# Performance work log

Measured on AMD Instinct MI355X. Metric: run time of the kernel, lower is better.

Reference implementation:

```python
import jax, jax.numpy as jnp
import numpy as np

B, Hh, Ww, E = 8, 32, 32, 256
HEADS = 8
KD = E // HEADS  # 32
FFN = 1024
NQ = 64
SCALING = KD ** -0.5
EPS = 1e-6


def _ln(x, g, b):
    m = x.mean(-1, keepdims=True)
    v = ((x - m) ** 2).mean(-1, keepdims=True)
    return (x - m) * jax.lax.rsqrt(v + EPS) * g + b


def _dwconv(x, w, b, pad):
    # x: (b,h,w,c); w: (c,1,kh,kw) depthwise
    y = jnp.transpose(x, (0, 3, 1, 2))
    y = jax.lax.conv_general_dilated(
        y, w, (1, 1), [(pad, pad), (pad, pad)],
        dimension_numbers=('NCHW', 'OIHW', 'NCHW'),
        feature_group_count=y.shape[1])
    y = y + b[None, :, None, None]
    return jnp.transpose(y, (0, 2, 3, 1))


def _rot2(x):
    x1 = x[..., ::2]
    x2 = x[..., 1::2]
    return jnp.stack([-x2, x1], axis=-1).reshape(x.shape)


def _theta_shift(x, sin, cos):
    return x * cos + _rot2(x) * sin


def _ffn(x, fc1_w, fc1_b, fc2_w, fc2_b):
    h = jax.nn.gelu(x @ fc1_w.T + fc1_b, approximate=False)
    return h @ fc2_w.T + fc2_b


def _mha(q, k, v, in_w, in_b, out_w, out_b):
    # torch nn.MultiheadAttention, batch_first=True
    wq, wk, wv = in_w[:E], in_w[E:2 * E], in_w[2 * E:]
    bq, bk, bv = in_b[:E], in_b[E:2 * E], in_b[2 * E:]
    b_, nq, _ = q.shape
    lk = k.shape[1]
    qp = (q @ wq.T + bq).reshape(b_, nq, HEADS, KD).transpose(0, 2, 1, 3)
    kp = (k @ wk.T + bk).reshape(b_, lk, HEADS, KD).transpose(0, 2, 1, 3)
    vp = (v @ wv.T + bv).reshape(b_, lk, HEADS, KD).transpose(0, 2, 1, 3)
    att = jax.nn.softmax(jnp.einsum('bhqd,bhkd->bhqk', qp, kp) * SCALING, axis=-1)
    out = jnp.einsum('bhqk,bhkd->bhqd', att, vp)
    out = out.transpose(0, 2, 1, 3).reshape(b_, nq, E)
    return out @ out_w.T + out_b


def setup_inputs() -> dict:
    key = jax.random.key(0)
    ks = jax.random.split(key, 24)
    n = lambda i, shp, s=1.0: jax.random.normal(ks[i], shp, jnp.float32) * s
    W = 0.02
    return {
        'x': n(0, (B, Hh, Ww, E)),
        'queries': n(1, (B, NQ, E)),
        'sin': n(2, (Hh, Ww, KD)),
        'cos': n(3, (Hh, Ww, KD)),
        'mask': n(4, (HEADS, Hh * Ww, Hh * Ww)),
        'ln1_g': jnp.ones((E,), jnp.float32), 'ln1_b': jnp.zeros((E,), jnp.float32),
        'ln2_g': jnp.ones((E,), jnp.float32), 'ln2_b': jnp.zeros((E,), jnp.float32),
        'wq': n(5, (E, E), W), 'bq': jnp.zeros((E,), jnp.float32),
        'wk': n(6, (E, E), W), 'bk': jnp.zeros((E,), jnp.float32),
        'wv': n(7, (E, E), W), 'bv': jnp.zeros((E,), jnp.float32),
        'lepe_w': n(8, (E, 1, 5, 5), W), 'lepe_b': jnp.zeros((E,), jnp.float32),
        'wo': n(9, (E, E), W), 'bo': jnp.zeros((E,), jnp.float32),
        'fc1_w': n(10, (FFN, E), W), 'fc1_b': jnp.zeros((FFN,), jnp.float32),
        'fc2_w': n(11, (E, FFN), W), 'fc2_b': jnp.zeros((E,), jnp.float32),
        'pos_w': n(12, (E, 1, 3, 3), W), 'pos_b': jnp.zeros((E,), jnp.float32),
        'ca_in_w': n(13, (3 * E, E), W), 'ca_in_b': jnp.zeros((3 * E,), jnp.float32),
        'ca_out_w': n(14, (E, E), W), 'ca_out_b': jnp.zeros((E,), jnp.float32),
    }


def reference(x, queries, sin, cos, mask, ln1_g, ln1_b, ln2_g, ln2_b,
              wq, bq, wk, bk, wv, bv, lepe_w, lepe_b, wo, bo,
              fc1_w, fc1_b, fc2_w, fc2_b, pos_w, pos_b,
              ca_in_w, ca_in_b, ca_out_w, ca_out_b):
    # conditional positional encoding
    x = x + _dwconv(x, pos_w, pos_b, 1)

    # --- retention branch (VisionRetentionAll) ---
    hn = _ln(x, ln1_g, ln1_b)
    q = hn @ wq.T + bq
    k = (hn @ wk.T + bk) * SCALING
    v = hn @ wv.T + bv
    lepe = _dwconv(v, lepe_w, lepe_b, 2)
    b_, hh, ww, _ = x.shape
    L = hh * ww
    qh = q.reshape(b_, hh, ww, HEADS, KD).transpose(0, 3, 1, 2, 4)
    kh = k.reshape(b_, hh, ww, HEADS, KD).transpose(0, 3, 1, 2, 4)
    qr = _theta_shift(qh, sin, cos).reshape(b_, HEADS, L, KD)
    kr = _theta_shift(kh, sin, cos).reshape(b_, HEADS, L, KD)
    vr = v.reshape(b_, hh, ww, HEADS, KD).transpose(0, 3, 1, 2, 4).reshape(b_, HEADS, L, KD)
    att = jax.nn.softmax(jnp.einsum('bnqd,bnkd->bnqk', qr, kr) + mask, axis=-1)
    out = jnp.einsum('bnqk,bnkd->bnqd', att, vr)
    out = out.transpose(0, 2, 1, 3).reshape(b_, hh, ww, E) + lepe
    x = x + (out @ wo.T + bo)

    # --- FFN branch ---
    x = x + _ffn(_ln(x, ln2_g, ln2_b), fc1_w, fc1_b, fc2_w, fc2_b)

    # --- cross-attention on queries ---
    xs = x.reshape(b_, L, E)
    q_ln = _ln(queries, ln1_g, ln1_b)
    queries = queries + _mha(q_ln, xs, xs, ca_in_w, ca_in_b, ca_out_w, ca_out_b)
    queries = queries + _ffn(_ln(queries, ln2_g, ln2_b), fc1_w, fc1_b, fc2_w, fc2_b)
    return x, queries
```

## Files before the change

kernel.cpp:

```cpp
#include <hip/hip_runtime.h>
#include <hip/hip_bf16.h>

#define B_      8
#define HH      32
#define WW      32
#define E_      256
#define HEADS_  8
#define KD_     32
#define FFN_    1024
#define NQ_     64
#define L_      1024
#define SCALING_ 0.17677669529663687f
#define LOG2E_  1.44269504088896340736f
#define EPS_    1e-6f

typedef short bf16x8 __attribute__((ext_vector_type(8)));
typedef float f32x4 __attribute__((ext_vector_type(4)));
typedef unsigned short ushort_t;

#if __has_builtin(__builtin_amdgcn_exp2f)
#define EXP2(x) __builtin_amdgcn_exp2f(x)
#else
#define EXP2(x) exp2f(x)
#endif

__device__ __forceinline__ ushort_t f2bf(float f) {
    __hip_bfloat16 h = __float2bfloat16(f);
    return *reinterpret_cast<ushort_t*>(&h);
}
__device__ __forceinline__ unsigned int pk2(float a, float b) {
    __hip_bfloat162 h = __float22bfloat162_rn(float2{a, b});
    return *reinterpret_cast<unsigned int*>(&h);
}

__global__ void dwT_kernel(const float* __restrict__ lepe_w, const float* __restrict__ pos_w,
                           float* __restrict__ LWT, float* __restrict__ PWT) {
    int e = threadIdx.x;
#pragma unroll
    for (int t = 0; t < 25; ++t) LWT[t * 256 + e] = lepe_w[e * 25 + t];
#pragma unroll
    for (int t = 0; t < 9; ++t) PWT[t * 256 + e] = pos_w[e * 9 + t];
}

__global__ __launch_bounds__(256) void posconv_ln2(
        const float* __restrict__ x, const float* __restrict__ PWT,
        const float* __restrict__ bias, const float* __restrict__ g,
        const float* __restrict__ bb, float* __restrict__ X, ushort_t* __restrict__ HN) {
    int tid = threadIdx.x;
    int wave = tid >> 6, lane = tid & 63;
    int b = blockIdx.x >> 8, rem = blockIdx.x & 255;
    int hh = rem >> 3, wg = rem & 7;
    int ww = wg * 4 + wave;
    int e = lane * 4;
    long row = ((long)(b * HH + hh)) * WW + ww;

    float4 bi = *reinterpret_cast<const float4*>(bias + e);
    float ax = bi.x, ay = bi.y, az = bi.z, aw = bi.w;
#pragma unroll
    for (int dh = 0; dh < 3; ++dh) {
        int h2 = hh + dh - 1; if (h2 < 0 || h2 >= HH) continue;
        float rx = 0.f, ry = 0.f, rz = 0.f, rw = 0.f;
#pragma unroll
        for (int dw = 0; dw < 3; ++dw) {
            int w2 = ww + dw - 1; if (w2 < 0 || w2 >= WW) continue;
            float4 v = *reinterpret_cast<const float4*>(x + (((long)(b * HH + h2)) * WW + w2) * E_ + e);
            float4 wt = *reinterpret_cast<const float4*>(PWT + (dh * 3 + dw) * 256 + e);
            rx += v.x * wt.x; ry += v.y * wt.y; rz += v.z * wt.z; rw += v.w * wt.w;
        }
        ax += rx; ay += ry; az += rz; aw += rw;
    }
    float4 x4 = *reinterpret_cast<const float4*>(x + row * E_ + e);
    float vx = x4.x + ax, vy = x4.y + ay, vz = x4.z + az, vw = x4.w + aw;
    float4 o4 = {vx, vy, vz, vw};
    *reinterpret_cast<float4*>(X + row * E_ + e) = o4;

    float s = vx + vy + vz + vw;
#pragma unroll
    for (int off = 1; off < 64; off <<= 1) s += __shfl_xor(s, off);
    float mean = s * (1.0f / E_);
    float dx = vx - mean, dy = vy - mean, dz = vz - mean, dw_ = vw - mean;
    float s2 = dx * dx + dy * dy + dz * dz + dw_ * dw_;
#pragma unroll
    for (int off = 1; off < 64; off <<= 1) s2 += __shfl_xor(s2, off);
    float r = rsqrtf(s2 * (1.0f / E_) + EPS_);
    float4 g4 = *reinterpret_cast<const float4*>(g + e);
    float4 b4 = *reinterpret_cast<const float4*>(bb + e);
    uint2 p;
    p.x = pk2(dx * r * g4.x + b4.x, dy * r * g4.y + b4.y);
    p.y = pk2(dz * r * g4.z + b4.z, dw_ * r * g4.w + b4.w);
    *reinterpret_cast<uint2*>(HN + row * E_ + e) = p;
}

__global__ __launch_bounds__(256) void lepe2(
        const float* __restrict__ v, const float* __restrict__ LWT,
        const float* __restrict__ bias, float* __restrict__ out) {
    int tid = threadIdx.x;
    int wave = tid >> 6, lane = tid & 63;
    int b = blockIdx.x >> 8, rem = blockIdx.x & 255;
    int hh = rem >> 3, wg = rem & 7;
    int ww = wg * 4 + wave;
    int e = lane * 4;
    long row = ((long)(b * HH + hh)) * WW + ww;

    float4 bi = *reinterpret_cast<const float4*>(bias + e);
    float ax = bi.x, ay = bi.y, az = bi.z, aw = bi.w;
#pragma unroll
    for (int dh = 0; dh < 5; ++dh) {
        int h2 = hh + dh - 2; if (h2 < 0 || h2 >= HH) continue;
        float rx = 0.f, ry = 0.f, rz = 0.f, rw = 0.f;
#pragma unroll
        for (int dw = 0; dw < 5; ++dw) {
            int w2 = ww + dw - 2; if (w2 < 0 || w2 >= WW) continue;
            float4 vv = *reinterpret_cast<const float4*>(v + (((long)(b * HH + h2)) * WW + w2) * E_ + e);
            float4 wt = *reinterpret_cast<const float4*>(LWT + (dh * 5 + dw) * 256 + e);
            rx += vv.x * wt.x; ry += vv.y * wt.y; rz += vv.z * wt.z; rw += vv.w * wt.w;
        }
        ax += rx; ay += ry; az += rz; aw += rw;
    }
    float4 o4 = {ax, ay, az, aw};
    *reinterpret_cast<float4*>(out + row * E_ + e) = o4;
}

__global__ __launch_bounds__(256) void ln2(
        const float* __restrict__ x, const float* __restrict__ g,
        const float* __restrict__ b, ushort_t* __restrict__ y) {
    int tid = threadIdx.x;
    int wave = tid >> 6, lane = tid & 63;
    long row = (long)blockIdx.x * 4 + wave;
    int e = lane * 4;
    float4 v4 = *reinterpret_cast<const float4*>(x + row * E_ + e);
    float s = v4.x + v4.y + v4.z + v4.w;
#pragma unroll
    for (int off = 1; off < 64; off <<= 1) s += __shfl_xor(s, off);
    float mean = s * (1.0f / E_);
    float dx = v4.x - mean, dy = v4.y - mean, dz = v4.z - mean, dw = v4.w - mean;
    float s2 = dx * dx + dy * dy + dz * dz + dw * dw;
#pragma unroll
    for (int off = 1; off < 64; off <<= 1) s2 += __shfl_xor(s2, off);
    float r = rsqrtf(s2 * (1.0f / E_) + EPS_);
    float4 g4 = *reinterpret_cast<const float4*>(g + e);
    float4 b4 = *reinterpret_cast<const float4*>(b + e);
    uint2 p;
    p.x = pk2(dx * r * g4.x + b4.x, dy * r * g4.y + b4.y);
    p.y = pk2(dz * r * g4.z + b4.z, dw * r * g4.w + b4.w);
    *reinterpret_cast<uint2*>(y + row * E_ + e) = p;
}

__global__ void maskcvt_kernel(const float* __restrict__ m, ushort_t* __restrict__ o) {
    long i = ((long)blockIdx.x * 256 + threadIdx.x) * 4;
    float4 v = *reinterpret_cast<const float4*>(m + i);
    uint2 p;
    p.x = pk2(v.x * LOG2E_, v.y * LOG2E_);
    p.y = pk2(v.z * LOG2E_, v.w * LOG2E_);
    *reinterpret_cast<uint2*>(o + i) = p;
}

struct WTab { const float* src[8]; };
__global__ void wconv_kernel(WTab t, ushort_t* __restrict__ dst) {
    const int off[9] = {0, 65536, 131072, 196608, 262144, 524288, 786432, 983040, 1048576};
    long base = ((long)blockIdx.x * 256 + threadIdx.x) * 4;
    int r = 0;
#pragma unroll
    for (int i = 1; i < 8; ++i) r = (base >= off[i]) ? i : r;
    const float* s =
        r == 0 ? t.src[0] : r == 1 ? t.src[1] : r == 2 ? t.src[2] : r == 3 ? t.src[3] :
        r == 4 ? t.src[4] : r == 5 ? t.src[5] : r == 6 ? t.src[6] : t.src[7];
    float4 v = *reinterpret_cast<const float4*>(s + (base - off[r]));
    uint2 p;
    p.x = pk2(v.x, v.y);
    p.y = pk2(v.z, v.w);
    *reinterpret_cast<uint2*>(dst + base) = p;
}

template<int ACT, int THETA>
__global__ __launch_bounds__(256) void gemm2(
        const ushort_t* __restrict__ A, const ushort_t* __restrict__ W,
        const float* __restrict__ bias, ushort_t* __restrict__ Cb,
        float* __restrict__ Cf, const float* __restrict__ resid,
        int M, int N, int K, float scale, int scaleN,
        const float* __restrict__ sinp, const float* __restrict__ cosp) {
    __shared__ __align__(16) ushort_t As[64 * 72];
    __shared__ __align__(16) ushort_t Ws[64 * 72];
    int tid = threadIdx.x;
    int wave = tid >> 6, lane = tid & 63;
    int quad = lane >> 4, l16 = lane & 15;
    int wm = wave >> 1, wn = wave & 1;
    long mBase = (long)blockIdx.x * 64;
    long nBase = (long)blockIdx.y * 64;
    int row = tid >> 3, q = tid & 7;
    int row2 = (tid + 256) >> 3, q2 = (tid + 256) & 7;

    f32x4 acc[2][2];
#pragma unroll
    for (int i = 0; i < 2; ++i)
#pragma unroll
        for (int j = 0; j < 2; ++j) acc[i][j] = (f32x4){0.f, 0.f, 0.f, 0.f};

    int nT = K >> 6;
    uint4 a0 = *reinterpret_cast<const uint4*>(A + (mBase + row) * (long)K + q * 8);
    uint4 a1 = *reinterpret_cast<const uint4*>(A + (mBase + row2) * (long)K + q2 * 8);
    uint4 w0 = *reinterpret_cast<const uint4*>(W + (nBase + row) * (long)K + q * 8);
    uint4 w1 = *reinterpret_cast<const uint4*>(W + (nBase + row2) * (long)K + q2 * 8);

    for (int t = 0; t < nT; ++t) {
        *reinterpret_cast<uint4*>(&As[row * 72 + q * 8]) = a0;
        *reinterpret_cast<uint4*>(&As[row2 * 72 + q2 * 8]) = a1;
        *reinterpret_cast<uint4*>(&Ws[row * 72 + q * 8]) = w0;
        *reinterpret_cast<uint4*>(&Ws[row2 * 72 + q2 * 8]) = w1;
        __syncthreads();
        if (t + 1 < nT) {
            int kt = (t + 1) << 6;
            a0 = *reinterpret_cast<const uint4*>(A + (mBase + row) * (long)K + kt + q * 8);
            a1 = *reinterpret_cast<const uint4*>(A + (mBase + row2) * (long)K + kt + q2 * 8);
            w0 = *reinterpret_cast<const uint4*>(W + (nBase + row) * (long)K + kt + q * 8);
            w1 = *reinterpret_cast<const uint4*>(W + (nBase + row2) * (long)K + kt + q2 * 8);
        }
#pragma unroll
        for (int kk = 0; kk < 2; ++kk) {
            bf16x8 af[2], bfr[2];
#pragma unroll
            for (int i = 0; i < 2; ++i)
                af[i] = *reinterpret_cast<const bf16x8*>(&As[(wm * 32 + i * 16 + l16) * 72 + kk * 32 + quad * 8]);
#pragma unroll
            for (int j = 0; j < 2; ++j)
                bfr[j] = *reinterpret_cast<const bf16x8*>(&Ws[(wn * 32 + j * 16 + l16) * 72 + kk * 32 + quad * 8]);
#pragma unroll
            for (int i = 0; i < 2; ++i)
#pragma unroll
                for (int j = 0; j < 2; ++j)
                    acc[i][j] = __builtin_amdgcn_mfma_f32_16x16x32_bf16(af[i], bfr[j], acc[i][j], 0, 0, 0);
        }
        __syncthreads();
    }

#pragma unroll
    for (int i = 0; i < 2; ++i)
#pragma unroll
        for (int j = 0; j < 2; ++j) {
            long n = nBase + wn * 32 + j * 16 + l16;
            float bn = bias[n];
            float eff = (n < scaleN) ? scale : 1.0f;
#pragma unroll
            for (int r = 0; r < 4; ++r) {
                long m = mBase + wm * 32 + i * 16 + quad * 4 + r;
                float v = (acc[i][j][r] + bn) * eff;
                if (THETA) {
                    float other = __shfl_xor(v, 1);
                    int l = (int)(m & (L_ - 1));
                    int d = (int)(n & 31);
                    float cc = cosp[l * 32 + d], ss = sinp[l * 32 + d];
                    v = v * cc + ((n & 1) ? other : -other) * ss;
                }
                if (ACT) v = 0.5f * v * (1.0f + erff(v * 0.70710678118654752f));
                if (resid) v += resid[m * N + n];
                if (Cf) Cf[m * N + n] = v;
                if (Cb) Cb[m * N + n] = f2bf(v);
            }
        }
}

__global__ __launch_bounds__(256) void attn4(
        const ushort_t* __restrict__ Q, int qs,
        const ushort_t* __restrict__ K, int ks,
        const ushort_t* __restrict__ V, int vs,
        const ushort_t* __restrict__ maskbf,
        const float* __restrict__ lepe, ushort_t* __restrict__ out, int nq) {
    __shared__ __align__(16) ushort_t Vt[2][32 * 136];
    __shared__ __align__(16) ushort_t Pl[4][16 * 136];
    int tid = threadIdx.x;
    int wave = tid >> 6, lane = tid & 63;
    int quad = lane >> 4, l16 = lane & 15;
    int qt = blockIdx.x, h = blockIdx.y, b = blockIdx.z;
    int qbase = qt * 64 + wave * 16;

    bf16x8 qfrag = *reinterpret_cast<const bf16x8*>(
        Q + ((long)b * nq + qbase + l16) * qs + h * KD_ + quad * 8);

    f32x4 acc_o[2];
    acc_o[0] = (f32x4){0.f, 0.f, 0.f, 0.f};
    acc_o[1] = (f32x4){0.f, 0.f, 0.f, 0.f};
    float lsum = 0.f;

    int kp = tid & 63;
    int dq = tid >> 6;

    const ushort_t* vp = V + ((long)b * L_ + 2 * kp) * vs + h * KD_ + dq * 8;
    uint4 ua = *reinterpret_cast<const uint4*>(vp);
    uint4 ub = *reinterpret_cast<const uint4*>(vp + vs);
    {
        const unsigned int* wa = reinterpret_cast<const unsigned int*>(&ua);
        const unsigned int* wb = reinterpret_cast<const unsigned int*>(&ub);
#pragma unroll
        for (int i = 0; i < 8; ++i) {
            unsigned int x16 = (wa[i >> 1] >> ((i & 1) * 16)) & 0xFFFF;
            unsigned int y16 = (wb[i >> 1] >> ((i & 1) * 16)) & 0xFFFF;
            *reinterpret_cast<unsigned int*>(&Vt[0][(dq * 8 + i) * 136 + 2 * kp]) =
                x16 | (y16 << 16);
        }
    }

    for (int it = 0; it < 8; ++it) {
        int kb = it * 128;
        __syncthreads();
        if (it < 7) {
            const ushort_t* vn = V + ((long)b * L_ + kb + 128 + 2 * kp) * vs + h * KD_ + dq * 8;
            ua = *reinterpret_cast<const uint4*>(vn);
            ub = *reinterpret_cast<const uint4*>(vn + vs);
        }
        uint2 mreg[8];
        if (maskbf) {
            const ushort_t* mb = maskbf + ((long)h * L_ + qbase + l16) * L_ + kb + quad * 4;
#pragma unroll
            for (int kt = 0; kt < 8; ++kt)
                mreg[kt] = *reinterpret_cast<const uint2*>(mb + kt * 16);
        }

#pragma unroll
        for (int g = 0; g < 2; ++g) {
            bf16x8 kf[4];
#pragma unroll
            for (int kt4 = 0; kt4 < 4; ++kt4)
                kf[kt4] = *reinterpret_cast<const bf16x8*>(
                    K + ((long)b * L_ + kb + (g * 4 + kt4) * 16 + l16) * ks + h * KD_ + quad * 8);
#pragma unroll
            for (int kt4 = 0; kt4 < 4; ++kt4) {
                int kt = g * 4 + kt4;
                f32x4 sa = (f32x4){0.f, 0.f, 0.f, 0.f};
                sa = __builtin_amdgcn_mfma_f32_16x16x32_bf16(kf[kt4], qfrag, sa, 0, 0, 0);
                float s0 = sa[0], s1 = sa[1], s2 = sa[2], s3 = sa[3];
                if (maskbf) {
                    s0 += __uint_as_float(mreg[kt].x << 16);
                    s1 += __uint_as_float(mreg[kt].x & 0xFFFF0000u);
                    s2 += __uint_as_float(mreg[kt].y << 16);
                    s3 += __uint_as_float(mreg[kt].y & 0xFFFF0000u);
                }
                float p0 = EXP2(s0), p1 = EXP2(s1), p2 = EXP2(s2), p3 = EXP2(s3);
                lsum += (p0 + p1) + (p2 + p3);
                uint2 pw;
                pw.x = pk2(p0, p1);
                pw.y = pk2(p2, p3);
                *reinterpret_cast<uint2*>(&Pl[wave][l16 * 136 + kt * 16 + quad * 4]) = pw;
            }
        }

#pragma unroll
        for (int c = 0; c < 4; ++c) {
            bf16x8 pa = *reinterpret_cast<const bf16x8*>(
                &Pl[wave][l16 * 136 + c * 32 + quad * 8]);
#pragma unroll
            for (int dt = 0; dt < 2; ++dt) {
                bf16x8 vf = *reinterpret_cast<const bf16x8*>(
                    &Vt[it & 1][(dt * 16 + l16) * 136 + c * 32 + quad * 8]);
                acc_o[dt] = __builtin_amdgcn_mfma_f32_16x16x32_bf16(pa, vf, acc_o[dt], 0, 0, 0);
            }
        }

        if (it < 7) {
            const unsigned int* wa = reinterpret_cast<const unsigned int*>(&ua);
            const unsigned int* wb = reinterpret_cast<const unsigned int*>(&ub);
#pragma unroll
            for (int i = 0; i < 8; ++i) {
                unsigned int x16 = (wa[i >> 1] >> ((i & 1) * 16)) & 0xFFFF;
                unsigned int y16 = (wb[i >> 1] >> ((i & 1) * 16)) & 0xFFFF;
                *reinterpret_cast<unsigned int*>(&Vt[(it + 1) & 1][(dq * 8 + i) * 136 + 2 * kp]) =
                    x16 | (y16 << 16);
            }
        }
    }

    lsum += __shfl_xor(lsum, 16);
    lsum += __shfl_xor(lsum, 32);
    float ls[4];
#pragma unroll
    for (int r = 0; r < 4; ++r) ls[r] = __shfl(lsum, quad * 4 + r);

#pragma unroll
    for (int dt = 0; dt < 2; ++dt)
#pragma unroll
        for (int r = 0; r < 4; ++r) {
            float v = acc_o[dt][r] / ls[r];
            long oi = ((long)b * nq + qbase + quad * 4 + r) * E_ + h * KD_ + dt * 16 + l16;
            if (lepe) v += lepe[oi];
            out[oi] = f2bf(v);
        }
}

extern "C" void kernel_launch(void* const* d_in, const int* in_sizes, int n_in,
                              void* d_out, int out_size, void* d_ws, size_t ws_size,
                              hipStream_t stream) {
    const float* x        = (const float*)d_in[0];
    const float* queries  = (const float*)d_in[1];
    const float* sinp     = (const float*)d_in[2];
    const float* cosp     = (const float*)d_in[3];
    const float* mask     = (const float*)d_in[4];
    const float* ln1_g    = (const float*)d_in[5];
    const float* ln1_b    = (const float*)d_in[6];
    const float* ln2_g    = (const float*)d_in[7];
    const float* ln2_b    = (const float*)d_in[8];
    const float* wq       = (const float*)d_in[9];
    const float* bq       = (const float*)d_in[10];
    const float* wk       = (const float*)d_in[11];
    const float* bk       = (const float*)d_in[12];
    const float* wv       = (const float*)d_in[13];
    const float* bv       = (const float*)d_in[14];
    const float* lepe_w   = (const float*)d_in[15];
    const float* lepe_b   = (const float*)d_in[16];
    const float* wo       = (const float*)d_in[17];
    const float* bo       = (const float*)d_in[18];
    const float* fc1_w    = (const float*)d_in[19];
    const float* fc1_b    = (const float*)d_in[20];
    const float* fc2_w    = (const float*)d_in[21];
    const float* fc2_b    = (const float*)d_in[22];
    const float* pos_w    = (const float*)d_in[23];
    const float* pos_b    = (const float*)d_in[24];
    const float* ca_in_w  = (const float*)d_in[25];
    const float* ca_in_b  = (const float*)d_in[26];
    const float* ca_out_w = (const float*)d_in[27];
    const float* ca_out_b = (const float*)d_in[28];

    float* ws = (float*)d_ws;
    const long SZ = (long)B_ * L_ * E_;
    float* X    = ws;
    float* Vbf  = ws + SZ;
    float* LEP  = ws + 2 * SZ;
    float* Q2   = LEP;
    ushort_t* U = (ushort_t*)(ws + 3 * SZ);
    ushort_t* T0    = U;
    ushort_t* Qb_u  = U + SZ;
    ushort_t* Kb_u  = U + 2 * SZ;
    ushort_t* Vb_u  = U + 3 * SZ;
    ushort_t* HID_u = U + 4 * SZ;
    ushort_t* MB_u  = HID_u;
    ushort_t* WB    = U + 8 * SZ;
    float* LWT      = (float*)(WB + 1048576);
    float* PWT      = LWT + 6400;
    ushort_t* KV_u   = U + SZ;
    ushort_t* QLN_u  = Vb_u;
    ushort_t* QP_u   = Vb_u + 131072;
    ushort_t* CAO_u  = Vb_u + 262144;
    ushort_t* QHID_u = Vb_u + 393216;
    ushort_t* wqB    = WB;
    ushort_t* wkB    = WB + 65536;
    ushort_t* wvB    = WB + 131072;
    ushort_t* woB    = WB + 196608;
    ushort_t* fc1B   = WB + 262144;
    ushort_t* fc2B   = WB + 524288;
    ushort_t* cainB  = WB + 786432;
    ushort_t* caoutB = WB + 983040;

    float* XOUT = (float*)d_out;
    float* QOUT = (float*)d_out + 2097152;

    dim3 blk(256);
    const int rows = B_ * L_;
    const float* Z = nullptr;
    const float KSCL = SCALING_ * LOG2E_;

    WTab wt;
    wt.src[0] = wq; wt.src[1] = wk; wt.src[2] = wv; wt.src[3] = wo;
    wt.src[4] = fc1_w; wt.src[5] = fc2_w; wt.src[6] = ca_in_w; wt.src[7] = ca_out_w;

    dwT_kernel<<<1, blk, 0, stream>>>(lepe_w, pos_w, LWT, PWT);
    wconv_kernel<<<1024, blk, 0, stream>>>(wt, WB);
    maskcvt_kernel<<<8192, blk, 0, stream>>>(mask, MB_u);
    posconv_ln2<<<2048, blk, 0, stream>>>(x, PWT, pos_b, ln1_g, ln1_b, X, T0);

    gemm2<0,1><<<dim3(128, 4), blk, 0, stream>>>(T0, wqB, bq, Qb_u, nullptr, Z, rows, 256, 256, 1.0f, 0, sinp, cosp);
    gemm2<0,1><<<dim3(128, 4), blk, 0, stream>>>(T0, wkB, bk, Kb_u, nullptr, Z, rows, 256, 256, KSCL, 256, sinp, cosp);
    gemm2<0,0><<<dim3(128, 4), blk, 0, stream>>>(T0, wvB, bv, Vb_u, Vbf, Z, rows, 256, 256, 1.0f, 0, Z, Z);
    lepe2<<<2048, blk, 0, stream>>>(Vbf, LWT, lepe_b, LEP);
    attn4<<<dim3(16, 8, 8), blk, 0, stream>>>(Qb_u, 256, Kb_u, 256, Vb_u, 256, MB_u, LEP, T0, L_);
    gemm2<0,0><<<dim3(128, 4), blk, 0, stream>>>(T0, woB, bo, nullptr, X, X, rows, 256, 256, 1.0f, 0, Z, Z);
    ln2<<<2048, blk, 0, stream>>>(X, ln2_g, ln2_b, T0);
    gemm2<1,0><<<dim3(128, 16), blk, 0, stream>>>(T0, fc1B, fc1_b, HID_u, nullptr, Z, rows, 1024, 256, 1.0f, 0, Z, Z);
    gemm2<0,0><<<dim3(128, 4), blk, 0, stream>>>(HID_u, fc2B, fc2_b, T0, XOUT, X, rows, 256, 1024, 1.0f, 0, Z, Z);

    ln2<<<128, blk, 0, stream>>>(queries, ln1_g, ln1_b, QLN_u);
    gemm2<0,0><<<dim3(8, 4), blk, 0, stream>>>(QLN_u, cainB, ca_in_b, QP_u, nullptr, Z, 512, 256, 256, 1.0f, 0, Z, Z);
    gemm2<0,0><<<dim3(128, 8), blk, 0, stream>>>(T0, cainB + 65536, ca_in_b + 256, KV_u, nullptr, Z, rows, 512, 256, KSCL, 256, Z, Z);
    attn4<<<dim3(1, 8, 8), blk, 0, stream>>>(QP_u, 256, KV_u, 512, KV_u + 256, 512, nullptr, nullptr, CAO_u, NQ_);
    gemm2<0,0><<<dim3(8, 4), blk, 0, stream>>>(CAO_u, caoutB, ca_out_b, nullptr, Q2, queries, 512, 256, 256, 1.0f, 0, Z, Z);
    ln2<<<128, blk, 0, stream>>>(Q2, ln2_g, ln2_b, QLN_u);
    gemm2<1,0><<<dim3(8, 16), blk, 0, stream>>>(QLN_u, fc1B, fc1_b, QHID_u, nullptr, Z, 512, 1024, 256, 1.0f, 0, Z, Z);
    gemm2<0,0><<<dim3(8, 4), blk, 0, stream>>>(QHID_u, fc2B, fc2_b, nullptr, QOUT, Q2, 512, 256, 1024, 1.0f, 0, Z, Z);
}
```

Before: 371.5 us.

## Fuse QKV projections, read fp32 mask directly in attention, merge prep kernels

```diff
diff --git a/kernel.cpp b/kernel.cpp
--- a/kernel.cpp
+++ b/kernel.cpp
@@ -33,15 +33,6 @@
     return *reinterpret_cast<unsigned int*>(&h);
 }
 
-__global__ void dwT_kernel(const float* __restrict__ lepe_w, const float* __restrict__ pos_w,
-                           float* __restrict__ LWT, float* __restrict__ PWT) {
-    int e = threadIdx.x;
-#pragma unroll
-    for (int t = 0; t < 25; ++t) LWT[t * 256 + e] = lepe_w[e * 25 + t];
-#pragma unroll
-    for (int t = 0; t < 9; ++t) PWT[t * 256 + e] = pos_w[e * 9 + t];
-}
-
 __global__ __launch_bounds__(256) void posconv_ln2(
         const float* __restrict__ x, const float* __restrict__ PWT,
         const float* __restrict__ bias, const float* __restrict__ g,
@@ -146,17 +137,18 @@
     *reinterpret_cast<uint2*>(y + row * E_ + e) = p;
 }
 
-__global__ void maskcvt_kernel(const float* __restrict__ m, ushort_t* __restrict__ o) {
-    long i = ((long)blockIdx.x * 256 + threadIdx.x) * 4;
-    float4 v = *reinterpret_cast<const float4*>(m + i);
-    uint2 p;
-    p.x = pk2(v.x * LOG2E_, v.y * LOG2E_);
-    p.y = pk2(v.z * LOG2E_, v.w * LOG2E_);
-    *reinterpret_cast<uint2*>(o + i) = p;
-}
-
 struct WTab { const float* src[8]; };
-__global__ void wconv_kernel(WTab t, ushort_t* __restrict__ dst) {
+__global__ void wconv_kernel(WTab t, ushort_t* __restrict__ dst,
+                             const float* __restrict__ lepe_w, const float* __restrict__ pos_w,
+                             float* __restrict__ LWT, float* __restrict__ PWT) {
+    if (blockIdx.x == 1024) {
+        int e = threadIdx.x;
+#pragma unroll
+        for (int tp = 0; tp < 25; ++tp) LWT[tp * 256 + e] = lepe_w[e * 25 + tp];
+#pragma unroll
+        for (int tp = 0; tp < 9; ++tp) PWT[tp * 256 + e] = pos_w[e * 9 + tp];
+        return;
+    }
     const int off[9] = {0, 65536, 131072, 196608, 262144, 524288, 786432, 983040, 1048576};
     long base = ((long)blockIdx.x * 256 + threadIdx.x) * 4;
     int r = 0;
@@ -259,11 +251,99 @@
         }
 }
 
-__global__ __launch_bounds__(256) void attn4(
+__global__ __launch_bounds__(256) void gemm_qkv3(
+        const ushort_t* __restrict__ A, const ushort_t* __restrict__ WB,
+        const float* __restrict__ bq, const float* __restrict__ bk, const float* __restrict__ bv,
+        ushort_t* __restrict__ Qb, ushort_t* __restrict__ Kb, ushort_t* __restrict__ Vb,
+        float* __restrict__ Vbf, const float* __restrict__ sinp,
+        const float* __restrict__ cosp, float kscl) {
+    __shared__ __align__(16) ushort_t As[64 * 72];
+    __shared__ __align__(16) ushort_t Ws[64 * 72];
+    int tid = threadIdx.x;
+    int wave = tid >> 6, lane = tid & 63;
+    int quad = lane >> 4, l16 = lane & 15;
+    int wm = wave >> 1, wn = wave & 1;
+    long mBase = (long)blockIdx.x * 64;
+    int sel = blockIdx.y >> 2;
+    int nLocBase = (blockIdx.y & 3) * 64;
+    const ushort_t* W = WB + ((long)(sel * 256 + nLocBase)) * 256;
+    const float* bias = sel == 0 ? bq : (sel == 1 ? bk : bv);
+    const int K = 256;
+    int row = tid >> 3, q = tid & 7;
+    int row2 = (tid + 256) >> 3, q2 = (tid + 256) & 7;
+
+    f32x4 acc[2][2];
+#pragma unroll
+    for (int i = 0; i < 2; ++i)
+#pragma unroll
+        for (int j = 0; j < 2; ++j) acc[i][j] = (f32x4){0.f, 0.f, 0.f, 0.f};
+
+    uint4 a0 = *reinterpret_cast<const uint4*>(A + (mBase + row) * (long)K + q * 8);
+    uint4 a1 = *reinterpret_cast<const uint4*>(A + (mBase + row2) * (long)K + q2 * 8);
+    uint4 w0 = *reinterpret_cast<const uint4*>(W + row * (long)K + q * 8);
+    uint4 w1 = *reinterpret_cast<const uint4*>(W + row2 * (long)K + q2 * 8);
+
+    for (int t = 0; t < 4; ++t) {
+        *reinterpret_cast<uint4*>(&As[row * 72 + q * 8]) = a0;
+        *reinterpret_cast<uint4*>(&As[row2 * 72 + q2 * 8]) = a1;
+        *reinterpret_cast<uint4*>(&Ws[row * 72 + q * 8]) = w0;
+        *reinterpret_cast<uint4*>(&Ws[row2 * 72 + q2 * 8]) = w1;
+        __syncthreads();
+        if (t < 3) {
+            int kt = (t + 1) << 6;
+            a0 = *reinterpret_cast<const uint4*>(A + (mBase + row) * (long)K + kt + q * 8);
+            a1 = *reinterpret_cast<const uint4*>(A + (mBase + row2) * (long)K + kt + q2 * 8);
+            w0 = *reinterpret_cast<const uint4*>(W + row * (long)K + kt + q * 8);
+            w1 = *reinterpret_cast<const uint4*>(W + row2 * (long)K + kt + q2 * 8);
+        }
+#pragma unroll
+        for (int kk = 0; kk < 2; ++kk) {
+            bf16x8 af[2], bfr[2];
+#pragma unroll
+            for (int i = 0; i < 2; ++i)
+                af[i] = *reinterpret_cast<const bf16x8*>(&As[(wm * 32 + i * 16 + l16) * 72 + kk * 32 + quad * 8]);
+#pragma unroll
+            for (int j = 0; j < 2; ++j)
+                bfr[j] = *reinterpret_cast<const bf16x8*>(&Ws[(wn * 32 + j * 16 + l16) * 72 + kk * 32 + quad * 8]);
+#pragma unroll
+            for (int i = 0; i < 2; ++i)
+#pragma unroll
+                for (int j = 0; j < 2; ++j)
+                    acc[i][j] = __builtin_amdgcn_mfma_f32_16x16x32_bf16(af[i], bfr[j], acc[i][j], 0, 0, 0);
+        }
+        __syncthreads();
+    }
+
+    ushort_t* Cb = sel == 0 ? Qb : (sel == 1 ? Kb : Vb);
+#pragma unroll
+    for (int i = 0; i < 2; ++i)
+#pragma unroll
+        for (int j = 0; j < 2; ++j) {
+            int n = nLocBase + wn * 32 + j * 16 + l16;
+            float bn = bias[n];
+#pragma unroll
+            for (int r = 0; r < 4; ++r) {
+                long m = mBase + wm * 32 + i * 16 + quad * 4 + r;
+                float v = acc[i][j][r] + bn;
+                if (sel == 1) v *= kscl;
+                if (sel < 2) {
+                    float other = __shfl_xor(v, 1);
+                    int l = (int)(m & (L_ - 1));
+                    int d = n & 31;
+                    float cc = cosp[l * 32 + d], ss = sinp[l * 32 + d];
+                    v = v * cc + ((n & 1) ? other : -other) * ss;
+                }
+                Cb[m * 256 + n] = f2bf(v);
+                if (sel == 2) Vbf[m * 256 + n] = v;
+            }
+        }
+}
+
+__global__ __launch_bounds__(256) void attn5(
         const ushort_t* __restrict__ Q, int qs,
         const ushort_t* __restrict__ K, int ks,
         const ushort_t* __restrict__ V, int vs,
-        const ushort_t* __restrict__ maskbf,
+        const float* __restrict__ maskf,
         const float* __restrict__ lepe, ushort_t* __restrict__ out, int nq) {
     __shared__ __align__(16) ushort_t Vt[2][32 * 136];
     __shared__ __align__(16) ushort_t Pl[4][16 * 136];
@@ -279,7 +359,7 @@
     f32x4 acc_o[2];
     acc_o[0] = (f32x4){0.f, 0.f, 0.f, 0.f};
     acc_o[1] = (f32x4){0.f, 0.f, 0.f, 0.f};
-    float lsum = 0.f;
+    float lsum[4] = {0.f, 0.f, 0.f, 0.f};
 
     int kp = tid & 63;
     int dq = tid >> 6;
@@ -307,39 +387,35 @@
             ua = *reinterpret_cast<const uint4*>(vn);
             ub = *reinterpret_cast<const uint4*>(vn + vs);
         }
-        uint2 mreg[8];
-        if (maskbf) {
-            const ushort_t* mb = maskbf + ((long)h * L_ + qbase + l16) * L_ + kb + quad * 4;
-#pragma unroll
-            for (int kt = 0; kt < 8; ++kt)
-                mreg[kt] = *reinterpret_cast<const uint2*>(mb + kt * 16);
-        }
 
 #pragma unroll
         for (int g = 0; g < 2; ++g) {
             bf16x8 kf[4];
+            float mr[4][4];
 #pragma unroll
             for (int kt4 = 0; kt4 < 4; ++kt4)
                 kf[kt4] = *reinterpret_cast<const bf16x8*>(
                     K + ((long)b * L_ + kb + (g * 4 + kt4) * 16 + l16) * ks + h * KD_ + quad * 8);
+            if (maskf) {
+#pragma unroll
+                for (int kt4 = 0; kt4 < 4; ++kt4)
+#pragma unroll
+                    for (int r = 0; r < 4; ++r)
+                        mr[kt4][r] = maskf[((long)h * L_ + qbase + quad * 4 + r) * L_ +
+                                           kb + (g * 4 + kt4) * 16 + l16];
+            }
 #pragma unroll
             for (int kt4 = 0; kt4 < 4; ++kt4) {
-                int kt = g * 4 + kt4;
+                int kcol = (g * 4 + kt4) * 16;
                 f32x4 sa = (f32x4){0.f, 0.f, 0.f, 0.f};
-                sa = __builtin_amdgcn_mfma_f32_16x16x32_bf16(kf[kt4], qfrag, sa, 0, 0, 0);
-                float s0 = sa[0], s1 = sa[1], s2 = sa[2], s3 = sa[3];
-                if (maskbf) {
-                    s0 += __uint_as_float(mreg[kt].x << 16);
-                    s1 += __uint_as_float(mreg[kt].x & 0xFFFF0000u);
-                    s2 += __uint_as_float(mreg[kt].y << 16);
-                    s3 += __uint_as_float(mreg[kt].y & 0xFFFF0000u);
+                sa = __builtin_amdgcn_mfma_f32_16x16x32_bf16(qfrag, kf[kt4], sa, 0, 0, 0);
+#pragma unroll
+                for (int r = 0; r < 4; ++r) {
+                    float s = maskf ? fmaf(mr[kt4][r], LOG2E_, sa[r]) : sa[r];
+                    float p = EXP2(s);
+                    lsum[r] += p;
+                    Pl[wave][(quad * 4 + r) * 136 + kcol + l16] = f2bf(p);
                 }
-                float p0 = EXP2(s0), p1 = EXP2(s1), p2 = EXP2(s2), p3 = EXP2(s3);
-                lsum += (p0 + p1) + (p2 + p3);
-                uint2 pw;
-                pw.x = pk2(p0, p1);
-                pw.y = pk2(p2, p3);
-                *reinterpret_cast<uint2*>(&Pl[wave][l16 * 136 + kt * 16 + quad * 4]) = pw;
             }
         }
 
@@ -368,17 +444,17 @@
         }
     }
 
-    lsum += __shfl_xor(lsum, 16);
-    lsum += __shfl_xor(lsum, 32);
-    float ls[4];
-#pragma unroll
-    for (int r = 0; r < 4; ++r) ls[r] = __shfl(lsum, quad * 4 + r);
+#pragma unroll
+    for (int off = 1; off < 16; off <<= 1) {
+#pragma unroll
+        for (int r = 0; r < 4; ++r) lsum[r] += __shfl_xor(lsum[r], off);
+    }
 
 #pragma unroll
     for (int dt = 0; dt < 2; ++dt)
 #pragma unroll
         for (int r = 0; r < 4; ++r) {
-            float v = acc_o[dt][r] / ls[r];
+            float v = acc_o[dt][r] / lsum[r];
             long oi = ((long)b * nq + qbase + quad * 4 + r) * E_ + h * KD_ + dt * 16 + l16;
             if (lepe) v += lepe[oi];
             out[oi] = f2bf(v);
@@ -430,7 +506,6 @@
     ushort_t* Kb_u  = U + 2 * SZ;
     ushort_t* Vb_u  = U + 3 * SZ;
     ushort_t* HID_u = U + 4 * SZ;
-    ushort_t* MB_u  = HID_u;
     ushort_t* WB    = U + 8 * SZ;
     float* LWT      = (float*)(WB + 1048576);
     float* PWT      = LWT + 6400;
@@ -440,8 +515,6 @@
     ushort_t* CAO_u  = Vb_u + 262144;
     ushort_t* QHID_u = Vb_u + 393216;
     ushort_t* wqB    = WB;
-    ushort_t* wkB    = WB + 65536;
-    ushort_t* wvB    = WB + 131072;
     ushort_t* woB    = WB + 196608;
     ushort_t* fc1B   = WB + 262144;
     ushort_t* fc2B   = WB + 524288;
@@ -460,16 +533,13 @@
     wt.src[0] = wq; wt.src[1] = wk; wt.src[2] = wv; wt.src[3] = wo;
     wt.src[4] = fc1_w; wt.src[5] = fc2_w; wt.src[6] = ca_in_w; wt.src[7] = ca_out_w;
 
-    dwT_kernel<<<1, blk, 0, stream>>>(lepe_w, pos_w, LWT, PWT);
-    wconv_kernel<<<1024, blk, 0, stream>>>(wt, WB);
-    maskcvt_kernel<<<8192, blk, 0, stream>>>(mask, MB_u);
+    wconv_kernel<<<1025, blk, 0, stream>>>(wt, WB, lepe_w, pos_w, LWT, PWT);
     posconv_ln2<<<2048, blk, 0, stream>>>(x, PWT, pos_b, ln1_g, ln1_b, X, T0);
 
-    gemm2<0,1><<<dim3(128, 4), blk, 0, stream>>>(T0, wqB, bq, Qb_u, nullptr, Z, rows, 256, 256, 1.0f, 0, sinp, cosp);
-    gemm2<0,1><<<dim3(128, 4), blk, 0, stream>>>(T0, wkB, bk, Kb_u, nullptr, Z, rows, 256, 256, KSCL, 256, sinp, cosp);
-    gemm2<0,0><<<dim3(128, 4), blk, 0, stream>>>(T0, wvB, bv, Vb_u, Vbf, Z, rows, 256, 256, 1.0f, 0, Z, Z);
+    gemm_qkv3<<<dim3(128, 12), blk, 0, stream>>>(T0, wqB, bq, bk, bv, Qb_u, Kb_u, Vb_u,
+                                                 Vbf, sinp, cosp, KSCL);
     lepe2<<<2048, blk, 0, stream>>>(Vbf, LWT, lepe_b, LEP);
-    attn4<<<dim3(16, 8, 8), blk, 0, stream>>>(Qb_u, 256, Kb_u, 256, Vb_u, 256, MB_u, LEP, T0, L_);
+    attn5<<<dim3(16, 8, 8), blk, 0, stream>>>(Qb_u, 256, Kb_u, 256, Vb_u, 256, mask, LEP, T0, L_);
     gemm2<0,0><<<dim3(128, 4), blk, 0, stream>>>(T0, woB, bo, nullptr, X, X, rows, 256, 256, 1.0f, 0, Z, Z);
     ln2<<<2048, blk, 0, stream>>>(X, ln2_g, ln2_b, T0);
     gemm2<1,0><<<dim3(128, 16), blk, 0, stream>>>(T0, fc1B, fc1_b, HID_u, nullptr, Z, rows, 1024, 256, 1.0f, 0, Z, Z);
@@ -478,7 +548,7 @@
     ln2<<<128, blk, 0, stream>>>(queries, ln1_g, ln1_b, QLN_u);
     gemm2<0,0><<<dim3(8, 4), blk, 0, stream>>>(QLN_u, cainB, ca_in_b, QP_u, nullptr, Z, 512, 256, 256, 1.0f, 0, Z, Z);
     gemm2<0,0><<<dim3(128, 8), blk, 0, stream>>>(T0, cainB + 65536, ca_in_b + 256, KV_u, nullptr, Z, rows, 512, 256, KSCL, 256, Z, Z);
-    attn4<<<dim3(1, 8, 8), blk, 0, stream>>>(QP_u, 256, KV_u, 512, KV_u + 256, 512, nullptr, nullptr, CAO_u, NQ_);
+    attn5<<<dim3(1, 8, 8), blk, 0, stream>>>(QP_u, 256, KV_u, 512, KV_u + 256, 512, Z, Z, CAO_u, NQ_);
     gemm2<0,0><<<dim3(8, 4), blk, 0, stream>>>(CAO_u, caoutB, ca_out_b, nullptr, Q2, queries, 512, 256, 256, 1.0f, 0, Z, Z);
     ln2<<<128, blk, 0, stream>>>(Q2, ln2_g, ln2_b, QLN_u);
     gemm2<1,0><<<dim3(8, 16), blk, 0, stream>>>(QLN_u, fc1B, fc1_b, QHID_u, nullptr, Z, 512, 1024, 256, 1.0f, 0, Z, Z);
```

After: 338.5 us. 8.9% less time.
